# Kernel optimization log

Hardware: AMD Instinct MI355X
Metric: run time of the kernel (lower is better)

Reference implementation:

```python
import jax, jax.numpy as jnp
import numpy as np

EMB = 1024
HEADS = 16
DK = EMB // HEADS
EPS = 1e-5


def setup_inputs() -> dict:
    key = jax.random.key(0)
    ks = jax.random.split(key, 7)
    s_in = 1.0 / np.sqrt(EMB)
    return {
        "x": jax.random.normal(ks[0], (4, 2048, EMB), dtype=jnp.float32),
        "W_qkv": jax.random.uniform(ks[1], (EMB, 3 * EMB), jnp.float32, -s_in, s_in),
        "b_qkv": jax.random.uniform(ks[2], (3 * EMB,), jnp.float32, -s_in, s_in),
        "W_out": jax.random.uniform(ks[3], (EMB, EMB), jnp.float32, -s_in, s_in),
        "b_out": jax.random.uniform(ks[4], (EMB,), jnp.float32, -s_in, s_in),
        "gamma": jnp.ones((EMB,), jnp.float32),
        "beta": jnp.zeros((EMB,), jnp.float32),
    }


def reference(x, W_qkv, b_qkv, W_out, b_out, gamma, beta):
    B, T, D = x.shape
    qkv = x @ W_qkv + b_qkv                      # [B,T,3D]
    q, k, v = jnp.split(qkv, 3, axis=-1)
    # [B,T,D] -> [B,H,T,dk]
    def heads(t):
        return t.reshape(B, T, HEADS, DK).transpose(0, 2, 1, 3)
    q, k, v = heads(q), heads(k), heads(v)
    scores = jnp.einsum("bhtd,bhsd->bhts", q, k) / np.sqrt(DK)
    attn = jax.nn.softmax(scores, axis=-1)
    out = jnp.einsum("bhts,bhsd->bhtd", attn, v)  # [B,H,T,dk]
    out = out.transpose(0, 2, 1, 3).reshape(B, T, D)
    out = out @ W_out + b_out
    res = x + out
    mu = jnp.mean(res, axis=-1, keepdims=True)
    var = jnp.mean((res - mu) ** 2, axis=-1, keepdims=True)
    return (res - mu) / jnp.sqrt(var + EPS) * gamma + beta
```

## Files before the change

### kernel.cpp

```cpp
#include <hip/hip_runtime.h>

#define B_ 4
#define T_ 2048
#define D_ 1024
#define H_ 16
#define DK_ 64
#define M_ (B_*T_)

typedef __bf16 bf16;
typedef __bf16 bf16x8 __attribute__((ext_vector_type(8)));
typedef __bf16 bf16x4 __attribute__((ext_vector_type(4)));
typedef short s16x4 __attribute__((ext_vector_type(4)));
typedef float f32x4 __attribute__((ext_vector_type(4)));

__device__ __forceinline__ f32x4 zero4() { f32x4 v = {0.f, 0.f, 0.f, 0.f}; return v; }

__device__ __forceinline__ float fexp2(float x) {
  float r;
  asm("v_exp_f32 %0, %1\n\ts_nop 0" : "=v"(r) : "v"(x));
  return r;
}

__device__ __forceinline__ float max3f(float a, float b, float c) {
  float r;
  asm("v_max3_f32 %0, %1, %2, %3" : "=v"(r) : "v"(a), "v"(b), "v"(c));
  return r;
}

__device__ __forceinline__ void g2l16(const void* g, void* l) {
  __builtin_amdgcn_global_load_lds(
      (const __attribute__((address_space(1))) void*)g,
      (__attribute__((address_space(3))) void*)l, 16, 0, 0);
}

__global__ __launch_bounds__(256) void prep(const float* __restrict__ x,
                                            const float* __restrict__ Wqkv,
                                            const float* __restrict__ Wout,
                                            bf16* __restrict__ xb,
                                            bf16* __restrict__ WqkvT,
                                            bf16* __restrict__ WoutT) {
  __shared__ alignas(16) bf16 ts[64 * 65];
  const int id = blockIdx.x;
  const int tid = threadIdx.x;
  if (id < 4096) {
    const size_t i = ((size_t)id * 256 + tid) * 8;
    float4 a = *(const float4*)(x + i);
    float4 b = *(const float4*)(x + i + 4);
    bf16x8 v;
    v[0] = (bf16)a.x; v[1] = (bf16)a.y; v[2] = (bf16)a.z; v[3] = (bf16)a.w;
    v[4] = (bf16)b.x; v[5] = (bf16)b.y; v[6] = (bf16)b.z; v[7] = (bf16)b.w;
    *(bf16x8*)(xb + i) = v;
    return;
  }
  const float* src; bf16* dst; int C, t;
  if (id < 4096 + 768) { t = id - 4096; src = Wqkv; dst = WqkvT; C = 3 * D_; }
  else                 { t = id - 4864; src = Wout; dst = WoutT; C = D_; }
  const int r0 = (t & 15) * 64, c0 = (t >> 4) * 64;
  {
    int rr = tid >> 2, cc = (tid & 3) * 16;
    const float4* p4 = (const float4*)(src + (size_t)(r0 + rr) * C + c0 + cc);
    float fv[16];
#pragma unroll
    for (int q = 0; q < 4; ++q) *(float4*)&fv[q * 4] = p4[q];
#pragma unroll
    for (int i = 0; i < 16; ++i) ts[(cc + i) * 65 + rr] = (bf16)fv[i];
  }
  __syncthreads();
  {
    int rr = tid >> 2, cc = (tid & 3) * 16;
    bf16x8 a, b;
#pragma unroll
    for (int i = 0; i < 8; ++i) a[i] = ts[rr * 65 + cc + i];
#pragma unroll
    for (int i = 0; i < 8; ++i) b[i] = ts[rr * 65 + cc + 8 + i];
    bf16* q = dst + (size_t)(c0 + rr) * D_ + r0 + cc;
    *(bf16x8*)q = a;
    *(bf16x8*)(q + 8) = b;
  }
}

template <bool FUSE>
__global__ __launch_bounds__(256) void gemm64(const bf16* __restrict__ A,
                                              const bf16* __restrict__ Bt,
                                              const float* __restrict__ bias,
                                              bf16* __restrict__ Cbf,
                                              float* __restrict__ Cf,
                                              const float* __restrict__ resid,
                                              int N, int K, int lda, int ldc) {
  __shared__ alignas(16) bf16 As[128 * 64];
  __shared__ alignas(16) bf16 Bs[128 * 64];
  const int tid = threadIdx.x;
  const int wid = tid >> 6, lane = tid & 63, quad = lane >> 4, l16 = lane & 15;
  const int w = (blockIdx.x & 7) * (gridDim.x >> 3) + (blockIdx.x >> 3);
  const int m0 = (w & 63) * 128, n0 = (w >> 6) * 128;
  const int wr = (wid >> 1) * 64, wc = (wid & 1) * 64;
  const int sw = l16 & 7;

  f32x4 acc[4][4];
#pragma unroll
  for (int i = 0; i < 4; ++i)
#pragma unroll
    for (int j = 0; j < 4; ++j) acc[i][j] = zero4();

  for (int k0 = 0; k0 < K; k0 += 64) {
    __syncthreads();
#pragma unroll
    for (int p = 0; p < 4; ++p) {
      const int t = p * 256 + tid;
      const int row = t >> 3;
      const int kcs = ((t & 7) ^ (row & 7)) * 8;
      g2l16(Bt + (size_t)(n0 + row) * K + k0 + kcs, (char*)Bs + p * 4096 + wid * 1024);
      g2l16(A + (size_t)(m0 + row) * lda + k0 + kcs, (char*)As + p * 4096 + wid * 1024);
    }
    __syncthreads();
#pragma unroll
    for (int kk = 0; kk < 2; ++kk) {
      bf16x8 af[4], bfr[4];
#pragma unroll
      for (int i = 0; i < 4; ++i)
        af[i] = *(const bf16x8*)&As[(wr + i * 16 + l16) * 64 + ((((kk << 2) | quad) ^ sw) * 8)];
#pragma unroll
      for (int j = 0; j < 4; ++j)
        bfr[j] = *(const bf16x8*)&Bs[(wc + j * 16 + l16) * 64 + ((((kk << 2) | quad) ^ sw) * 8)];
#pragma unroll
      for (int i = 0; i < 4; ++i)
#pragma unroll
        for (int j = 0; j < 4; ++j)
          acc[i][j] = __builtin_amdgcn_mfma_f32_16x16x32_bf16(af[i], bfr[j], acc[i][j], 0, 0, 0);
    }
  }

#pragma unroll
  for (int i = 0; i < 4; ++i) {
#pragma unroll
    for (int j = 0; j < 4; ++j) {
      const int col = n0 + wc + j * 16 + l16;
      const float bv = bias[col];
#pragma unroll
      for (int r = 0; r < 4; ++r) {
        const int row = m0 + wr + i * 16 + quad * 4 + r;
        const float v = acc[i][j][r] + bv;
        if (FUSE) {
          const size_t off = (size_t)row * N + col;
          Cf[off] = v + resid[off];
        } else {
          Cbf[(size_t)row * ldc + col] = (bf16)v;
        }
      }
    }
  }
}

__global__ __launch_bounds__(256, 4) void attn_db(const bf16* __restrict__ qkv,
                                                  bf16* __restrict__ ao) {
  __shared__ alignas(16) bf16 Ks[2][4096];
  __shared__ alignas(16) bf16 Vs2[2][4096];
  const int tid = threadIdx.x;
  const int wid = tid >> 6, lane = tid & 63, quad = lane >> 4, l16 = lane & 15;
  const int bid0 = blockIdx.x;
  const int bid = ((bid0 & 7) << 7) | (bid0 >> 3);
  const int qb = bid & 15, h = (bid >> 4) & 15, b = bid >> 8;
  const int q0 = qb * 128;

  const int lrow8 = lane >> 3;
  const int kch = (lane & 7) ^ lrow8;
  const bf16* kg = qkv + (size_t)(b * T_ + wid * 16 + lrow8) * (3 * D_) + D_ + h * DK_ + kch * 8;
  const int vtok = wid * 8 + (lane >> 5) * 4 + ((lane >> 1) & 3);
  const int vfof = ((lane >> 3) & 3) * 16 + (lane & 1) * 8;
  const bf16* vg = qkv + (size_t)(b * T_ + vtok) * (3 * D_) + 2 * D_ + h * DK_ + vfof;
  const unsigned vbase = (unsigned)(uintptr_t)&Vs2[0][0];

  const float SC = 0.125f * 1.44269504f;
  bf16x8 qA[2], qB[2];
  {
    const bf16* qpA = qkv + (size_t)(b * T_ + q0 + wid * 32 + l16) * (3 * D_) + h * DK_ + quad * 8;
    const bf16* qpB = qpA + (size_t)16 * (3 * D_);
    qA[0] = *(const bf16x8*)qpA;       qA[1] = *(const bf16x8*)(qpA + 32);
    qB[0] = *(const bf16x8*)qpB;       qB[1] = *(const bf16x8*)(qpB + 32);
#pragma unroll
    for (int i = 0; i < 8; ++i) {
      qA[0][i] = (bf16)((float)qA[0][i] * SC); qA[1][i] = (bf16)((float)qA[1][i] * SC);
      qB[0][i] = (bf16)((float)qB[0][i] * SC); qB[1][i] = (bf16)((float)qB[1][i] * SC);
    }
  }

  float miA = -1e30f, miB = -1e30f;
  f32x4 liA4 = zero4(), liB4 = zero4();
  f32x4 oA[4], oB[4];
#pragma unroll
  for (int ft = 0; ft < 4; ++ft) { oA[ft] = zero4(); oB[ft] = zero4(); }

  auto stage = [&](int buf, int t0) {
    g2l16(kg + (size_t)(t0 + 0) * (3 * D_), &Ks[buf][(wid * 16 + 0) * 64]);
    g2l16(kg + (size_t)(t0 + 8) * (3 * D_), &Ks[buf][(wid * 16 + 8) * 64]);
    g2l16(vg + (size_t)(t0 + 0) * (3 * D_),  (char*)&Vs2[buf][0] + (0 + wid * 2) * 512);
    g2l16(vg + (size_t)(t0 + 32) * (3 * D_), (char*)&Vs2[buf][0] + (8 + wid * 2) * 512);
  };

  stage(0, 0);
  __syncthreads();

  for (int kt = 0; kt < T_ / 64; ++kt) {
    const int cur = kt & 1;
    if (kt + 1 < T_ / 64) stage(cur ^ 1, (kt + 1) * 64);

    f32x4 svA[4], svB[4];
#pragma unroll
    for (int nt = 0; nt < 4; ++nt) { svA[nt] = zero4(); svB[nt] = zero4(); }
    __builtin_amdgcn_s_setprio(1);
#pragma unroll
    for (int nt = 0; nt < 4; ++nt)
#pragma unroll
      for (int ks = 0; ks < 2; ++ks) {
        const bf16x8 kf = *(const bf16x8*)
            &Ks[cur][(nt * 16 + l16) * 64 + (((ks << 2) | quad) ^ (l16 & 7)) * 8];
        svA[nt] = __builtin_amdgcn_mfma_f32_16x16x32_bf16(kf, qA[ks], svA[nt], 0, 0, 0);
        svB[nt] = __builtin_amdgcn_mfma_f32_16x16x32_bf16(kf, qB[ks], svB[nt], 0, 0, 0);
      }
    __builtin_amdgcn_s_setprio(0);

    float a0 = max3f(svA[0][0], svA[0][1], svA[0][2]);
    float a1 = max3f(svA[0][3], svA[1][0], svA[1][1]);
    a0 = max3f(a0, svA[1][2], svA[1][3]);
    a1 = max3f(a1, svA[2][0], svA[2][1]);
    a0 = max3f(a0, svA[2][2], svA[2][3]);
    a1 = max3f(a1, svA[3][0], svA[3][1]);
    a0 = max3f(a0, svA[3][2], svA[3][3]);
    float b0 = max3f(svB[0][0], svB[0][1], svB[0][2]);
    float b1 = max3f(svB[0][3], svB[1][0], svB[1][1]);
    b0 = max3f(b0, svB[1][2], svB[1][3]);
    b1 = max3f(b1, svB[2][0], svB[2][1]);
    b0 = max3f(b0, svB[2][2], svB[2][3]);
    b1 = max3f(b1, svB[3][0], svB[3][1]);
    b0 = max3f(b0, svB[3][2], svB[3][3]);
    const float tAl = fmaxf(a0, a1), tBl = fmaxf(b0, b1);

    if (!__all(tAl <= miA + 8.f)) {
      float tA = fmaxf(tAl, __shfl_xor(tAl, 16, 64));
      tA = fmaxf(tA, __shfl_xor(tA, 32, 64));
      const float nm = fmaxf(miA, tA);
      const float al = fexp2(miA - nm);
      miA = nm; liA4 *= al;
#pragma unroll
      for (int r = 0; r < 4; ++r) {
        const float ar = __shfl(al, quad * 4 + r, 64);
#pragma unroll
        for (int ft = 0; ft < 4; ++ft) oA[ft][r] *= ar;
      }
    }
    if (!__all(tBl <= miB + 8.f)) {
      float tB = fmaxf(tBl, __shfl_xor(tBl, 16, 64));
      tB = fmaxf(tB, __shfl_xor(tB, 32, 64));
      const float nm = fmaxf(miB, tB);
      const float al = fexp2(miB - nm);
      miB = nm; liB4 *= al;
#pragma unroll
      for (int r = 0; r < 4; ++r) {
        const float ar = __shfl(al, quad * 4 + r, 64);
#pragma unroll
        for (int ft = 0; ft < 4; ++ft) oB[ft][r] *= ar;
      }
    }

    s16x4 pA[4], pB[4];
#pragma unroll
    for (int nt = 0; nt < 4; ++nt) {
      f32x4 dA = svA[nt] - miA;
      dA[0] = fexp2(dA[0]); dA[1] = fexp2(dA[1]); dA[2] = fexp2(dA[2]); dA[3] = fexp2(dA[3]);
      liA4 += dA;
      union { bf16x4 b; s16x4 s; } ua;
#pragma unroll
      for (int j = 0; j < 4; ++j) ua.b[j] = (bf16)dA[j];
      pA[nt] = ua.s;
      f32x4 dB = svB[nt] - miB;
      dB[0] = fexp2(dB[0]); dB[1] = fexp2(dB[1]); dB[2] = fexp2(dB[2]); dB[3] = fexp2(dB[3]);
      liB4 += dB;
      union { bf16x4 b; s16x4 s; } ub;
#pragma unroll
      for (int j = 0; j < 4; ++j) ub.b[j] = (bf16)dB[j];
      pB[nt] = ub.s;
    }

    __builtin_amdgcn_s_setprio(1);
    {
      const unsigned va = vbase + (unsigned)cur * 8192u + (unsigned)(quad * 512 + l16 * 8);
#pragma unroll
      for (int ks = 0; ks < 4; ++ks) {
        s16x4 vf[4];
#pragma unroll
        for (int ft = 0; ft < 4; ++ft)
          asm volatile("ds_read_b64_tr_b16 %0, %1 offset:%2"
                       : "=v"(vf[ft]) : "v"(va), "i"(ks * 2048 + ft * 128));
        asm volatile("s_waitcnt lgkmcnt(0)" ::: "memory");
        __builtin_amdgcn_sched_barrier(0);
#pragma unroll
        for (int ft = 0; ft < 4; ++ft) {
          oA[ft] = __builtin_amdgcn_mfma_f32_16x16x16bf16_1k(pA[ks], vf[ft], oA[ft], 0, 0, 0);
          oB[ft] = __builtin_amdgcn_mfma_f32_16x16x16bf16_1k(pB[ks], vf[ft], oB[ft], 0, 0, 0);
        }
      }
    }
    __builtin_amdgcn_s_setprio(0);

    __syncthreads();
  }

  float sA = (liA4[0] + liA4[1]) + (liA4[2] + liA4[3]);
  sA += __shfl_xor(sA, 16, 64);
  sA += __shfl_xor(sA, 32, 64);
  float sB = (liB4[0] + liB4[1]) + (liB4[2] + liB4[3]);
  sB += __shfl_xor(sB, 16, 64);
  sB += __shfl_xor(sB, 32, 64);

#pragma unroll
  for (int r = 0; r < 4; ++r) {
    const float invA = 1.0f / __shfl(sA, quad * 4 + r, 64);
    const float invB = 1.0f / __shfl(sB, quad * 4 + r, 64);
    const int rowA = b * T_ + q0 + wid * 32 + quad * 4 + r;
    const int rowB = rowA + 16;
#pragma unroll
    for (int ft = 0; ft < 4; ++ft) {
      ao[(size_t)rowA * D_ + h * DK_ + ft * 16 + l16] = (bf16)(oA[ft][r] * invA);
      ao[(size_t)rowB * D_ + h * DK_ + ft * 16 + l16] = (bf16)(oB[ft][r] * invB);
    }
  }
}

__global__ __launch_bounds__(256) void ln_out(float* __restrict__ res,
                                              const float* __restrict__ gamma,
                                              const float* __restrict__ beta) {
  const int row = blockIdx.x * 4 + (threadIdx.x >> 6);
  const int lane = threadIdx.x & 63;
  float4 v[4];
  float s = 0.f, q = 0.f;
#pragma unroll
  for (int p = 0; p < 4; ++p) {
    v[p] = *(const float4*)(res + (size_t)row * D_ + p * 256 + lane * 4);
    s += v[p].x + v[p].y + v[p].z + v[p].w;
    q += v[p].x * v[p].x + v[p].y * v[p].y + v[p].z * v[p].z + v[p].w * v[p].w;
  }
#pragma unroll
  for (int m = 1; m < 64; m <<= 1) { s += __shfl_xor(s, m, 64); q += __shfl_xor(q, m, 64); }
  const float mu = s * (1.0f / D_);
  const float var = q * (1.0f / D_) - mu * mu;
  const float rstd = rsqrtf(var + 1e-5f);
#pragma unroll
  for (int p = 0; p < 4; ++p) {
    const int c = p * 256 + lane * 4;
    const float4 g = *(const float4*)(gamma + c);
    const float4 be = *(const float4*)(beta + c);
    float4 ov;
    ov.x = (v[p].x - mu) * rstd * g.x + be.x;
    ov.y = (v[p].y - mu) * rstd * g.y + be.y;
    ov.z = (v[p].z - mu) * rstd * g.z + be.z;
    ov.w = (v[p].w - mu) * rstd * g.w + be.w;
    *(float4*)(res + (size_t)row * D_ + c) = ov;
  }
}

extern "C" void kernel_launch(void* const* d_in, const int* in_sizes, int n_in,
                              void* d_out, int out_size, void* d_ws, size_t ws_size,
                              hipStream_t stream) {
  const float* x     = (const float*)d_in[0];
  const float* Wqkv  = (const float*)d_in[1];
  const float* bqkv  = (const float*)d_in[2];
  const float* Wout  = (const float*)d_in[3];
  const float* bout  = (const float*)d_in[4];
  const float* gamma = (const float*)d_in[5];
  const float* beta  = (const float*)d_in[6];
  float* out = (float*)d_out;

  char* ws = (char*)d_ws;
  bf16* WqkvT = (bf16*)ws; ws += (size_t)3 * D_ * D_ * 2;
  bf16* WoutT = (bf16*)ws; ws += (size_t)D_ * D_ * 2;
  bf16* qkv   = (bf16*)ws; ws += (size_t)M_ * 3 * D_ * 2;
  bf16* ao    = (bf16*)ws;
  bf16* xb    = ao;

  prep<<<4096 + 768 + 256, 256, 0, stream>>>(x, Wqkv, Wout, xb, WqkvT, WoutT);
  gemm64<false><<<(M_ / 128) * (3 * D_ / 128), 256, 0, stream>>>(
      xb, WqkvT, bqkv, qkv, nullptr, nullptr, 3 * D_, D_, D_, 3 * D_);
  attn_db<<<B_ * H_ * (T_ / 128), 256, 0, stream>>>(qkv, ao);
  gemm64<true><<<(M_ / 128) * (D_ / 128), 256, 0, stream>>>(
      ao, WoutT, bout, nullptr, out, x, D_, D_, D_, D_);
  ln_out<<<M_ / 4, 256, 0, stream>>>(out, gamma, beta);
}
```

Baseline: 304.8 us.

## Software-pipeline QK^T of next tile ahead of PV with triple-buffered K

Restructures the attention loop so the QK^T MFMAs for the next key tile are issued after the softmax of the current tile and before its PV MFMAs. K is now triple-buffered and prefetched two tiles ahead, while V stays double-buffered one tile ahead. The goal is to overlap the exp/softmax VALU work with matrix-core work and hide more load latency. In exchange it uses 8 KB more LDS per block and keeps the score registers live longer, which may reduce occupancy at 4 blocks per CU.

New measurement: 303.3 us. About the same (-0.5%).

```diff
diff --git a/kernel.cpp b/kernel.cpp
--- a/kernel.cpp
+++ b/kernel.cpp
@@ -153,7 +153,7 @@
 
 __global__ __launch_bounds__(256, 4) void attn_db(const bf16* __restrict__ qkv,
                                                   bf16* __restrict__ ao) {
-  __shared__ alignas(16) bf16 Ks[2][4096];
+  __shared__ alignas(16) bf16 Ks[3][4096];
   __shared__ alignas(16) bf16 Vs2[2][4096];
   const int tid = threadIdx.x;
   const int wid = tid >> 6, lane = tid & 63, quad = lane >> 4, l16 = lane & 15;
@@ -190,21 +190,17 @@
 #pragma unroll
   for (int ft = 0; ft < 4; ++ft) { oA[ft] = zero4(); oB[ft] = zero4(); }
 
-  auto stage = [&](int buf, int t0) {
-    g2l16(kg + (size_t)(t0 + 0) * (3 * D_), &Ks[buf][(wid * 16 + 0) * 64]);
-    g2l16(kg + (size_t)(t0 + 8) * (3 * D_), &Ks[buf][(wid * 16 + 8) * 64]);
-    g2l16(vg + (size_t)(t0 + 0) * (3 * D_),  (char*)&Vs2[buf][0] + (0 + wid * 2) * 512);
-    g2l16(vg + (size_t)(t0 + 32) * (3 * D_), (char*)&Vs2[buf][0] + (8 + wid * 2) * 512);
+  auto stageK = [&](int kb, int t0) {
+    g2l16(kg + (size_t)(t0 + 0) * (3 * D_), &Ks[kb][(wid * 16 + 0) * 64]);
+    g2l16(kg + (size_t)(t0 + 8) * (3 * D_), &Ks[kb][(wid * 16 + 8) * 64]);
   };
-
-  stage(0, 0);
-  __syncthreads();
-
-  for (int kt = 0; kt < T_ / 64; ++kt) {
-    const int cur = kt & 1;
-    if (kt + 1 < T_ / 64) stage(cur ^ 1, (kt + 1) * 64);
-
-    f32x4 svA[4], svB[4];
+  auto stageV = [&](int vb, int t0) {
+    g2l16(vg + (size_t)(t0 + 0) * (3 * D_),  (char*)&Vs2[vb][0] + (0 + wid * 2) * 512);
+    g2l16(vg + (size_t)(t0 + 32) * (3 * D_), (char*)&Vs2[vb][0] + (8 + wid * 2) * 512);
+  };
+
+  f32x4 svA[4], svB[4];
+  auto qk = [&](const bf16* Kb) {
 #pragma unroll
     for (int nt = 0; nt < 4; ++nt) { svA[nt] = zero4(); svB[nt] = zero4(); }
     __builtin_amdgcn_s_setprio(1);
@@ -213,11 +209,23 @@
 #pragma unroll
       for (int ks = 0; ks < 2; ++ks) {
         const bf16x8 kf = *(const bf16x8*)
-            &Ks[cur][(nt * 16 + l16) * 64 + (((ks << 2) | quad) ^ (l16 & 7)) * 8];
+            &Kb[(nt * 16 + l16) * 64 + (((ks << 2) | quad) ^ (l16 & 7)) * 8];
         svA[nt] = __builtin_amdgcn_mfma_f32_16x16x32_bf16(kf, qA[ks], svA[nt], 0, 0, 0);
         svB[nt] = __builtin_amdgcn_mfma_f32_16x16x32_bf16(kf, qB[ks], svB[nt], 0, 0, 0);
       }
     __builtin_amdgcn_s_setprio(0);
+  };
+
+  stageK(0, 0); stageV(0, 0);
+  stageK(1, 64);
+  __syncthreads();
+  qk(&Ks[0][0]);
+
+  const int NT = T_ / 64;
+  int kbQ = 1, kbS = 2;
+  for (int kt = 0; kt < NT; ++kt) {
+    if (kt + 2 < NT) stageK(kbS, (kt + 2) * 64);
+    if (kt + 1 < NT) stageV((kt + 1) & 1, (kt + 1) * 64);
 
     float a0 = max3f(svA[0][0], svA[0][1], svA[0][2]);
     float a1 = max3f(svA[0][3], svA[1][0], svA[1][1]);
@@ -281,9 +289,11 @@
       pB[nt] = ub.s;
     }
 
+    if (kt + 1 < NT) qk(&Ks[kbQ][0]);
+
     __builtin_amdgcn_s_setprio(1);
     {
-      const unsigned va = vbase + (unsigned)cur * 8192u + (unsigned)(quad * 512 + l16 * 8);
+      const unsigned va = vbase + (unsigned)(kt & 1) * 8192u + (unsigned)(quad * 512 + l16 * 8);
 #pragma unroll
       for (int ks = 0; ks < 4; ++ks) {
         s16x4 vf[4];
@@ -303,6 +313,8 @@
     __builtin_amdgcn_s_setprio(0);
 
     __syncthreads();
+    const int old = 3 - kbQ - kbS;
+    kbQ = kbS; kbS = old;
   }
 
   float sA = (liA4[0] + liA4[1]) + (liA4[2] + liA4[3]);
```
